# Kernel tuning notes

Measured on AMD Instinct MI355X. Metric: run time of the kernel, lower is better.

Reference implementation:

```python
import jax, jax.numpy as jnp
import numpy as np

N_NODES = 10000
N_EDGES = 160000
IN_CH = 256
HIDDEN = 512
N_LAYERS = 2
W_SCALE = 0.05  # keep relu chain numerically tame


def setup_inputs() -> dict:
    key = jax.random.key(0)
    ks = jax.random.split(key, 8)
    x = jax.random.normal(ks[0], (N_NODES, IN_CH), dtype=jnp.float32)
    edge_index = jax.random.randint(ks[1], (2, N_EDGES), 0, N_NODES, dtype=jnp.int64)
    W_in = jax.random.normal(ks[2], (IN_CH, HIDDEN), dtype=jnp.float32) * W_SCALE
    b_in = jnp.zeros((HIDDEN,), jnp.float32)
    msg_W = jax.random.normal(ks[3], (N_LAYERS, HIDDEN, HIDDEN), dtype=jnp.float32) * W_SCALE
    msg_b = jnp.zeros((N_LAYERS, HIDDEN), jnp.float32)
    upd_W = jax.random.normal(ks[4], (N_LAYERS, 2 * HIDDEN, HIDDEN), dtype=jnp.float32) * W_SCALE
    upd_b = jnp.zeros((N_LAYERS, HIDDEN), jnp.float32)
    W_out = jax.random.normal(ks[5], (HIDDEN, 1), dtype=jnp.float32) * W_SCALE
    b_out = jnp.zeros((1,), jnp.float32)
    return {"x": x, "edge_index": edge_index, "W_in": W_in, "b_in": b_in,
            "msg_W": msg_W, "msg_b": msg_b, "upd_W": upd_W, "upd_b": upd_b,
            "W_out": W_out, "b_out": b_out}


def reference(x, edge_index, W_in, b_in, msg_W, msg_b, upd_W, upd_b, W_out, b_out):
    src = edge_index[0]  # x_j source nodes (PyG source_to_target flow)
    dst = edge_index[1]  # aggregate into destination nodes
    n = x.shape[0]
    h = jax.nn.relu(x @ W_in + b_in)  # [N, H]
    for l in range(msg_W.shape[0]):
        # message: relu(Linear(x_j)) on gathered source features  [E, H]
        m = jax.nn.relu(h[src] @ msg_W[l] + msg_b[l])
        # aggr='add': scatter-add over destination nodes  [N, H]
        aggr = jax.ops.segment_sum(m, dst, num_segments=n)
        # update: relu(Linear(concat([x, aggr])))  [N, H]
        h = jax.nn.relu(jnp.concatenate([h, aggr], axis=-1) @ upd_W[l] + upd_b[l])
    out = h @ W_out + b_out  # [N, 1]
    return out.squeeze(-1)
```

## Files before the change

kernel.cpp:

```cpp
#include <hip/hip_runtime.h>


typedef _Float16 half8 __attribute__((ext_vector_type(8)));
typedef float float4v __attribute__((ext_vector_type(4)));

#define ASYNC_COPY16(gptr, lptr)                                              \
    __builtin_amdgcn_global_load_lds(                                         \
        (const __attribute__((address_space(1))) void*)(gptr),                \
        (__attribute__((address_space(3))) void*)(lptr), 16, 0, 0)


__device__ __forceinline__ void gemm_body(int id,
    const _Float16* __restrict__ A1, int KT1,
    const _Float16* __restrict__ A2, int KT2,
    const _Float16* __restrict__ Wt, int KTw, int ktw2,
    const float* __restrict__ bias, _Float16* __restrict__ C,
    int M, int Mtiles, int packC, int do_relu,
    const float* __restrict__ Wout, const float* __restrict__ bout,
    float* __restrict__ outp)
{
    __shared__ _Float16 As[4096];
    __shared__ _Float16 Bs[4096];

    const int tid  = threadIdx.x;
    const int wave = tid >> 6, lane = tid & 63;

    const int cxcd = id & 7, j = id >> 3;
    const int mt = cxcd + 8 * (j >> 3);
    if (mt >= Mtiles) return;
    const int pn = j & 7;
    const int bm = mt * 64, bn = pn * 64;

    const int wr = (wave >> 1) * 32, wc = (wave & 1) * 32;
    const int m16 = lane & 15, quad = lane >> 4;

    float4v acc[2][2] = {};
    float bv[2];
    #pragma unroll
    for (int jj = 0; jj < 2; ++jj) bv[jj] = bias[bn + wc + jj * 16 + m16];

    for (int pass = 0; pass < 2; ++pass) {
        const _Float16* __restrict__ A = pass ? A2 : A1;
        if (A == nullptr) continue;
        const int KTa  = pass ? KT2 : KT1;
        const int ktw0 = pass ? ktw2 : 0;

        for (int kt = 0; kt < KTa; ++kt) {
            const _Float16* Ab = A  + (size_t)(mt * KTa + kt) * 4096;
            const _Float16* Wb = Wt + (size_t)(pn * KTw + ktw0 + kt) * 4096;
            #pragma unroll
            for (int t = 0; t < 2; ++t) {
                const int q = t * 4 + wave;
                ASYNC_COPY16(Ab + q * 512 + lane * 8, (char*)As + q * 1024);
                ASYNC_COPY16(Wb + q * 512 + lane * 8, (char*)Bs + q * 1024);
            }
            __syncthreads();
            #pragma unroll
            for (int c = 0; c < 2; ++c) {
                half8 af[2], bf[2];
                #pragma unroll
                for (int i2 = 0; i2 < 2; ++i2)
                    af[i2] = *(const half8*)
                        &As[((c * 4 + quad) * 64 + wr + i2 * 16 + m16) * 8];
                #pragma unroll
                for (int j2 = 0; j2 < 2; ++j2)
                    bf[j2] = *(const half8*)
                        &Bs[((c * 4 + quad) * 64 + wc + j2 * 16 + m16) * 8];
                #pragma unroll
                for (int i2 = 0; i2 < 2; ++i2)
                    #pragma unroll
                    for (int j2 = 0; j2 < 2; ++j2)
                        acc[i2][j2] = __builtin_amdgcn_mfma_f32_16x16x32_f16(
                            af[i2], bf[j2], acc[i2][j2], 0, 0, 0);
            }
            __syncthreads();
        }
    }

    if (outp) {
        #pragma unroll
        for (int i = 0; i < 2; ++i)
            #pragma unroll
            for (int rg = 0; rg < 4; ++rg) {
                const int r2 = wr + i * 16 + quad * 4 + rg;
                const int row = bm + r2;
                float pr = 0.f;
                #pragma unroll
                for (int j2 = 0; j2 < 2; ++j2) {
                    float v = fmaxf(acc[i][j2][rg] + bv[j2], 0.f);
                    pr += v * Wout[bn + wc + j2 * 16 + m16];
                }
                pr += __shfl_xor(pr, 1);
                pr += __shfl_xor(pr, 2);
                pr += __shfl_xor(pr, 4);
                pr += __shfl_xor(pr, 8);
                if (m16 == 0 && row < M)
                    atomicAdd(&outp[row],
                              pr + ((pn == 0 && wc == 0) ? bout[0] : 0.f));
            }
        return;
    }

    #pragma unroll
    for (int i = 0; i < 2; ++i)
        #pragma unroll
        for (int rg = 0; rg < 4; ++rg) {
            const int r2 = wr + i * 16 + quad * 4 + rg;
            const int row = bm + r2;
            if (row >= M) continue;
            #pragma unroll
            for (int j2 = 0; j2 < 2; ++j2) {
                float v = acc[i][j2][rg] + bv[j2];
                if (do_relu) v = fmaxf(v, 0.f);
                const int coff = wc + j2 * 16 + m16;
                if (packC) {
                    C[(size_t)((mt * 8 + pn) * 8 + (coff >> 3)) * 512
                      + r2 * 8 + (coff & 7)] = (_Float16)v;
                } else {
                    C[(size_t)row * 512 + bn + coff] = (_Float16)v;
                }
            }
        }
}

__global__ __launch_bounds__(256) void gemm_f16(
    const _Float16* __restrict__ A1, int KT1,
    const _Float16* __restrict__ A2, int KT2,
    const _Float16* __restrict__ Wt, int KTw, int ktw2,
    const float* __restrict__ bias, _Float16* __restrict__ C,
    int M, int Mtiles, int packC, int do_relu,
    const float* Wout, const float* bout, float* outp)
{
    gemm_body(blockIdx.x, A1, KT1, A2, KT2, Wt, KTw, ktw2,
              bias, C, M, Mtiles, packC, do_relu, Wout, bout, outp);
}

__device__ __forceinline__ void transpose_unit(
    const float* __restrict__ src, _Float16* __restrict__ dst, int R, int tb)
{
    const int rtiles = R >> 5;
    const int r0 = (tb % rtiles) * 32, c0 = (tb / rtiles) * 32;
    const int KT = R >> 6;
    __shared__ float t[32][33];
    const int tid = threadIdx.x;
    const int tx = tid & 31, ty = tid >> 5;
    #pragma unroll
    for (int i = 0; i < 32; i += 8)
        t[ty + i][tx] = src[(size_t)(r0 + ty + i) * 512 + c0 + tx];
    __syncthreads();
    if (tid < 128) {
        const int n  = c0 + (tid >> 2);
        const int k0 = r0 + (tid & 3) * 8;
        half8 o;
        #pragma unroll
        for (int j2 = 0; j2 < 8; ++j2)
            o[j2] = (_Float16)t[(tid & 3) * 8 + j2][tid >> 2];
        *(half8*)&dst[(size_t)(((n >> 6) * KT + (k0 >> 6)) * 8 + ((k0 >> 3) & 7)) * 512
                      + (n & 63) * 8] = o;
    }
}

__global__ __launch_bounds__(256) void fill_ingemm(
    const int* __restrict__ eidx, int* __restrict__ cursor,
    int* __restrict__ srcs, int E,
    const _Float16* __restrict__ xb, const _Float16* __restrict__ WinT,
    const float* __restrict__ b_in, _Float16* __restrict__ B0,
    int M, int Mtiles,
    const float* __restrict__ msg_W, _Float16* __restrict__ msgT,
    const float* __restrict__ upd_W, _Float16* __restrict__ updT)
{
    const int gemmU = ((Mtiles + 7) >> 3) * 64;
    const int fillU = (E + 255) >> 8;
    const int b = blockIdx.x;
    if (b < gemmU) {
        gemm_body(b, xb, 4, nullptr, 0, WinT, 4, 0,
                  b_in, B0, M, Mtiles, 1, 1, nullptr, nullptr, nullptr);
        return;
    }
    if (b < gemmU + fillU) {
        const int e = (b - gemmU) * 256 + threadIdx.x;
        if (e < E) {
            const int d = eidx[E + e];
            const int pos = atomicAdd(&cursor[d], 1);
            if (pos < 64) srcs[d * 64 + pos] = eidx[e];
        }
        return;
    }
    const int tB = b - gemmU - fillU;
    if (tB < 256)       transpose_unit(msg_W,              msgT,              512,  tB);
    else if (tB < 512)  transpose_unit(msg_W + 512 * 512,  msgT + 512 * 512,  512,  tB - 256);
    else if (tB < 1024) transpose_unit(upd_W,              updT,              1024, tB - 512);
    else                transpose_unit(upd_W + 1024 * 512, updT + 512 * 1024, 1024, tB - 1024);
}

__global__ __launch_bounds__(256) void prep(
    const float* __restrict__ W_in,  _Float16* __restrict__ WinT,
    const float* __restrict__ x,     _Float16* __restrict__ xb,
    int* __restrict__ cursor, float* __restrict__ outz,
    int n4, int M)
{
    const int b = blockIdx.x;
    const int tid = threadIdx.x;
    const int castU = (n4 + 255) >> 8;
    if (b < 128) {
        transpose_unit(W_in, WinT, 256, b);
    } else if (b < 128 + castU) {
        const int i = (b - 128) * 256 + tid;
        if (i < n4) {
            const float4 v = *(const float4*)(x + (size_t)i * 4);
            ushort4 s;
            union { _Float16 h; unsigned short u; } cv;
            cv.h = (_Float16)v.x; s.x = cv.u;
            cv.h = (_Float16)v.y; s.y = cv.u;
            cv.h = (_Float16)v.z; s.z = cv.u;
            cv.h = (_Float16)v.w; s.w = cv.u;
            const int f = i * 4;
            const int m = f >> 8, k = f & 255;
            *(ushort4*)((unsigned short*)xb
                + (size_t)(((m >> 6) * 4 + (k >> 6)) * 8 + ((k >> 3) & 7)) * 512
                + (m & 63) * 8 + (k & 7)) = s;
        }
    } else {
        const int zi = (b - 128 - castU) * 256 + tid;
        if (zi < M) { cursor[zi] = 0; outz[zi] = 0.f; }
    }
}

__global__ __launch_bounds__(256) void aggregate_f16(
    const _Float16* __restrict__ hmr, const int* __restrict__ cursor,
    const int* __restrict__ srcs, _Float16* __restrict__ ag, int n)
{
    const int l16  = threadIdx.x & 15;
    const int node = blockIdx.x * 16 + (threadIdx.x >> 4);
    if (node >= n) return;
    const int c8 = blockIdx.y * 128 + l16 * 8;
    const int beg = node * 64;
    const int end = beg + min(cursor[node], 64);
    float a[8] = {};
    int j = beg;
    for (; j + 3 < end; j += 4) {
        const half8 v0 = *(const half8*)(hmr + (size_t)srcs[j]     * 512 + c8);
        const half8 v1 = *(const half8*)(hmr + (size_t)srcs[j + 1] * 512 + c8);
        const half8 v2 = *(const half8*)(hmr + (size_t)srcs[j + 2] * 512 + c8);
        const half8 v3 = *(const half8*)(hmr + (size_t)srcs[j + 3] * 512 + c8);
        #pragma unroll
        for (int i = 0; i < 8; ++i)
            a[i] += ((float)v0[i] + (float)v1[i]) + ((float)v2[i] + (float)v3[i]);
    }
    for (; j < end; ++j) {
        const half8 v = *(const half8*)(hmr + (size_t)srcs[j] * 512 + c8);
        #pragma unroll
        for (int i = 0; i < 8; ++i) a[i] += (float)v[i];
    }
    half8 o;
    #pragma unroll
    for (int i = 0; i < 8; ++i) o[i] = (_Float16)a[i];
    *(half8*)(ag + (size_t)(((node >> 6) * 8 + (c8 >> 6)) * 8 + ((c8 >> 3) & 7)) * 512
              + (node & 63) * 8) = o;
}

extern "C" void kernel_launch(void* const* d_in, const int* in_sizes, int n_in,
                              void* d_out, int out_size, void* d_ws, size_t ws_size,
                              hipStream_t stream)
{
    const float* x     = (const float*)d_in[0];
    const int*   eidx  = (const int*)  d_in[1];
    const float* W_in  = (const float*)d_in[2];
    const float* b_in  = (const float*)d_in[3];
    const float* msg_W = (const float*)d_in[4];
    const float* msg_b = (const float*)d_in[5];
    const float* upd_W = (const float*)d_in[6];
    const float* upd_b = (const float*)d_in[7];
    const float* W_out = (const float*)d_in[8];
    const float* b_out = (const float*)d_in[9];

    const int IN = 256, H = 512;
    const int M = in_sizes[0] / IN;
    const int E = in_sizes[1] / 2;
    const int Mtiles = (M + 63) / 64;
    const size_t Mt64 = (size_t)Mtiles * 64;

    _Float16* xb   = (_Float16*)d_ws;
    _Float16* B0   = xb + Mt64 * IN;
    _Float16* B1   = B0 + Mt64 * H;
    _Float16* B2   = B1 + Mt64 * H;
    _Float16* WinT = B2 + Mt64 * H;
    _Float16* msgT = WinT + (size_t)H * IN;
    _Float16* updT = msgT + (size_t)2 * H * H;
    int* cursor = (int*)(updT + (size_t)2 * H * 2 * H);
    int* srcs   = cursor + M;

    const dim3 blk(256);
    const int gemmBlocks = ((Mtiles + 7) / 8) * 64;
    const dim3 aggrGrid((M + 15) / 16, 4);

    const int n4 = M * IN / 4;
    const int castU = (n4 + 255) / 256;
    const int fillU = (E + 255) / 256;
    const int zeroU = (M + 255) / 256;
    const int transU = 1536;

    prep<<<dim3(128 + castU + zeroU), blk, 0, stream>>>(
        W_in, WinT, x, xb, cursor, (float*)d_out, n4, M);
    fill_ingemm<<<dim3(gemmBlocks + fillU + transU), blk, 0, stream>>>(
        eidx, cursor, srcs, E, xb, WinT, b_in, B0, M, Mtiles,
        msg_W, msgT, upd_W, updT);

    gemm_f16<<<dim3(gemmBlocks), blk, 0, stream>>>(B0, 8, nullptr, 0,
        msgT, 8, 0, msg_b, B1, M, Mtiles, 0, 1,
        nullptr, nullptr, nullptr);
    aggregate_f16<<<aggrGrid, blk, 0, stream>>>(B1, cursor, srcs, B2, M);
    gemm_f16<<<dim3(gemmBlocks), blk, 0, stream>>>(B0, 8, B2, 8,
        updT, 16, 8, upd_b, B1, M, Mtiles, 1, 1,
        nullptr, nullptr, nullptr);
    gemm_f16<<<dim3(gemmBlocks), blk, 0, stream>>>(B1, 8, nullptr, 0,
        msgT + 512 * 512, 8, 0, msg_b + 512, B0, M, Mtiles, 0, 1,
        nullptr, nullptr, nullptr);
    aggregate_f16<<<aggrGrid, blk, 0, stream>>>(B0, cursor, srcs, B2, M);
    gemm_f16<<<dim3(gemmBlocks), blk, 0, stream>>>(B1, 8, B2, 8,
        updT + 512 * 1024, 16, 8, upd_b + 512, nullptr, M, Mtiles, 1, 1,
        W_out, b_out, (float*)d_out);
}
```

Measured before the change: 201.3 us.

## Grow GEMM tile to 128x64 and XOR-swizzle packed fp16 layout

The GEMM block tile doubles from 64x64 to 128x64, with each wave computing 32x64 so every B fragment is reused across more rows. All producers of the packed tile layout (transpose, x cast, aggregation, GEMM packed output) now XOR-swizzle the row index by the k-chunk to cut LDS bank conflicts on fragment reads. The aim is less LDS traffic and more MFMA work per byte loaded. In exchange it doubles the accumulator registers and A LDS footprint, halves the number of blocks, and drops the row<M bound check on packed stores, which depends on padded buffers.

```diff
diff --git a/kernel.cpp b/kernel.cpp
--- a/kernel.cpp
+++ b/kernel.cpp
@@ -19,7 +19,7 @@
     const float* __restrict__ Wout, const float* __restrict__ bout,
     float* __restrict__ outp)
 {
-    __shared__ _Float16 As[4096];
+    __shared__ _Float16 As[8192];
     __shared__ _Float16 Bs[4096];
 
     const int tid  = threadIdx.x;
@@ -29,15 +29,17 @@
     const int mt = cxcd + 8 * (j >> 3);
     if (mt >= Mtiles) return;
     const int pn = j & 7;
-    const int bm = mt * 64, bn = pn * 64;
-
-    const int wr = (wave >> 1) * 32, wc = (wave & 1) * 32;
+    const int bm = mt * 128, bn = pn * 64;
+
+    const int wr  = wave * 32;
     const int m16 = lane & 15, quad = lane >> 4;
-
-    float4v acc[2][2] = {};
-    float bv[2];
+    const int sub = wave >> 1;
+    const int rb  = (wave & 1) * 32;
+
+    float4v acc[2][4] = {};
+    float bv[4];
     #pragma unroll
-    for (int jj = 0; jj < 2; ++jj) bv[jj] = bias[bn + wc + jj * 16 + m16];
+    for (int jj = 0; jj < 4; ++jj) bv[jj] = bias[bn + jj * 16 + m16];
 
     for (int pass = 0; pass < 2; ++pass) {
         const _Float16* __restrict__ A = pass ? A2 : A1;
@@ -46,30 +48,33 @@
         const int ktw0 = pass ? ktw2 : 0;
 
         for (int kt = 0; kt < KTa; ++kt) {
-            const _Float16* Ab = A  + (size_t)(mt * KTa + kt) * 4096;
-            const _Float16* Wb = Wt + (size_t)(pn * KTw + ktw0 + kt) * 4096;
+            const _Float16* Ab0 = A + (size_t)((2 * mt)     * KTa + kt) * 4096;
+            const _Float16* Ab1 = A + (size_t)((2 * mt + 1) * KTa + kt) * 4096;
+            const _Float16* Wb  = Wt + (size_t)(pn * KTw + ktw0 + kt) * 4096;
             #pragma unroll
             for (int t = 0; t < 2; ++t) {
                 const int q = t * 4 + wave;
-                ASYNC_COPY16(Ab + q * 512 + lane * 8, (char*)As + q * 1024);
-                ASYNC_COPY16(Wb + q * 512 + lane * 8, (char*)Bs + q * 1024);
+                ASYNC_COPY16(Ab0 + q * 512 + lane * 8, (char*)As + q * 1024);
+                ASYNC_COPY16(Ab1 + q * 512 + lane * 8, (char*)As + 8192 + q * 1024);
+                ASYNC_COPY16(Wb  + q * 512 + lane * 8, (char*)Bs + q * 1024);
             }
             __syncthreads();
             #pragma unroll
             for (int c = 0; c < 2; ++c) {
-                half8 af[2], bf[2];
+                const int ch = c * 4 + quad;
+                half8 af[2], bf[4];
                 #pragma unroll
                 for (int i2 = 0; i2 < 2; ++i2)
                     af[i2] = *(const half8*)
-                        &As[((c * 4 + quad) * 64 + wr + i2 * 16 + m16) * 8];
+                        &As[sub * 4096 + (ch * 64 + ((rb + i2 * 16 + m16) ^ ch)) * 8];
                 #pragma unroll
-                for (int j2 = 0; j2 < 2; ++j2)
+                for (int j2 = 0; j2 < 4; ++j2)
                     bf[j2] = *(const half8*)
-                        &Bs[((c * 4 + quad) * 64 + wc + j2 * 16 + m16) * 8];
+                        &Bs[(ch * 64 + ((j2 * 16 + m16) ^ ch)) * 8];
                 #pragma unroll
                 for (int i2 = 0; i2 < 2; ++i2)
                     #pragma unroll
-                    for (int j2 = 0; j2 < 2; ++j2)
+                    for (int j2 = 0; j2 < 4; ++j2)
                         acc[i2][j2] = __builtin_amdgcn_mfma_f32_16x16x32_f16(
                             af[i2], bf[j2], acc[i2][j2], 0, 0, 0);
             }
@@ -86,17 +91,16 @@
                 const int row = bm + r2;
                 float pr = 0.f;
                 #pragma unroll
-                for (int j2 = 0; j2 < 2; ++j2) {
+                for (int j2 = 0; j2 < 4; ++j2) {
                     float v = fmaxf(acc[i][j2][rg] + bv[j2], 0.f);
-                    pr += v * Wout[bn + wc + j2 * 16 + m16];
+                    pr += v * Wout[bn + j2 * 16 + m16];
                 }
                 pr += __shfl_xor(pr, 1);
                 pr += __shfl_xor(pr, 2);
                 pr += __shfl_xor(pr, 4);
                 pr += __shfl_xor(pr, 8);
                 if (m16 == 0 && row < M)
-                    atomicAdd(&outp[row],
-                              pr + ((pn == 0 && wc == 0) ? bout[0] : 0.f));
+                    atomicAdd(&outp[row], pr + (pn == 0 ? bout[0] : 0.f));
             }
         return;
     }
@@ -107,15 +111,14 @@
         for (int rg = 0; rg < 4; ++rg) {
             const int r2 = wr + i * 16 + quad * 4 + rg;
             const int row = bm + r2;
-            if (row >= M) continue;
             #pragma unroll
-            for (int j2 = 0; j2 < 2; ++j2) {
+            for (int j2 = 0; j2 < 4; ++j2) {
                 float v = acc[i][j2][rg] + bv[j2];
                 if (do_relu) v = fmaxf(v, 0.f);
-                const int coff = wc + j2 * 16 + m16;
+                const int coff = j2 * 16 + m16;
                 if (packC) {
-                    C[(size_t)((mt * 8 + pn) * 8 + (coff >> 3)) * 512
-                      + r2 * 8 + (coff & 7)] = (_Float16)v;
+                    C[(size_t)(((mt * 2 + (r2 >> 6)) * 8 + pn) * 8 + (coff >> 3)) * 512
+                      + ((r2 & 63) ^ (coff >> 3)) * 8 + (coff & 7)] = (_Float16)v;
                 } else {
                     C[(size_t)row * 512 + bn + coff] = (_Float16)v;
                 }
@@ -156,7 +159,7 @@
         for (int j2 = 0; j2 < 8; ++j2)
             o[j2] = (_Float16)t[(tid & 3) * 8 + j2][tid >> 2];
         *(half8*)&dst[(size_t)(((n >> 6) * KT + (k0 >> 6)) * 8 + ((k0 >> 3) & 7)) * 512
-                      + (n & 63) * 8] = o;
+                      + ((n & 63) ^ ((k0 >> 3) & 7)) * 8] = o;
     }
 }
 
@@ -218,7 +221,7 @@
             const int m = f >> 8, k = f & 255;
             *(ushort4*)((unsigned short*)xb
                 + (size_t)(((m >> 6) * 4 + (k >> 6)) * 8 + ((k >> 3) & 7)) * 512
-                + (m & 63) * 8 + (k & 7)) = s;
+                + ((m & 63) ^ ((k >> 3) & 7)) * 8 + (k & 7)) = s;
         }
     } else {
         const int zi = (b - 128 - castU) * 256 + tid;
@@ -256,7 +259,7 @@
     #pragma unroll
     for (int i = 0; i < 8; ++i) o[i] = (_Float16)a[i];
     *(half8*)(ag + (size_t)(((node >> 6) * 8 + (c8 >> 6)) * 8 + ((c8 >> 3) & 7)) * 512
-              + (node & 63) * 8) = o;
+              + ((node & 63) ^ ((c8 >> 3) & 7)) * 8) = o;
 }
 
 extern "C" void kernel_launch(void* const* d_in, const int* in_sizes, int n_in,
@@ -277,14 +280,14 @@
     const int IN = 256, H = 512;
     const int M = in_sizes[0] / IN;
     const int E = in_sizes[1] / 2;
-    const int Mtiles = (M + 63) / 64;
-    const size_t Mt64 = (size_t)Mtiles * 64;
+    const int Mtiles = (M + 127) / 128;
+    const size_t Mt = (size_t)Mtiles * 128;
 
     _Float16* xb   = (_Float16*)d_ws;
-    _Float16* B0   = xb + Mt64 * IN;
-    _Float16* B1   = B0 + Mt64 * H;
-    _Float16* B2   = B1 + Mt64 * H;
-    _Float16* WinT = B2 + Mt64 * H;
+    _Float16* B0   = xb + Mt * IN;
+    _Float16* B1   = B0 + Mt * H;
+    _Float16* B2   = B1 + Mt * H;
+    _Float16* WinT = B2 + Mt * H;
     _Float16* msgT = WinT + (size_t)H * IN;
     _Float16* updT = msgT + (size_t)2 * H * H;
     int* cursor = (int*)(updT + (size_t)2 * H * 2 * H);
```

Measured after the change: 204.7 us. About the same (+1.7%).

## Double-buffer LDS tiles in GEMM to overlap async loads with MFMA

Applied to the files above, without the earlier changes.

Doubles the LDS A/B buffers and restructures the K loop so the next tile's async global-to-LDS copies are issued before computing on the current tile, waiting on vmcnt(4) so only the older loads must land. The two-pass loop over A1/A2 is flattened into one unified tile index. This targets the exposed global load latency at every K step, at the cost of twice the LDS per block, which may reduce occupancy, and of relying on hand-written waitcnt counts.

```diff
diff --git a/kernel.cpp b/kernel.cpp
--- a/kernel.cpp
+++ b/kernel.cpp
@@ -19,8 +19,8 @@
     const float* __restrict__ Wout, const float* __restrict__ bout,
     float* __restrict__ outp)
 {
-    __shared__ _Float16 As[4096];
-    __shared__ _Float16 Bs[4096];
+    __shared__ _Float16 As[8192];
+    __shared__ _Float16 Bs[8192];
 
     const int tid  = threadIdx.x;
     const int wave = tid >> 6, lane = tid & 63;
@@ -39,42 +39,60 @@
     #pragma unroll
     for (int jj = 0; jj < 2; ++jj) bv[jj] = bias[bn + wc + jj * 16 + m16];
 
-    for (int pass = 0; pass < 2; ++pass) {
-        const _Float16* __restrict__ A = pass ? A2 : A1;
-        if (A == nullptr) continue;
-        const int KTa  = pass ? KT2 : KT1;
-        const int ktw0 = pass ? ktw2 : 0;
-
-        for (int kt = 0; kt < KTa; ++kt) {
-            const _Float16* Ab = A  + (size_t)(mt * KTa + kt) * 4096;
-            const _Float16* Wb = Wt + (size_t)(pn * KTw + ktw0 + kt) * 4096;
-            #pragma unroll
-            for (int t = 0; t < 2; ++t) {
-                const int q = t * 4 + wave;
-                ASYNC_COPY16(Ab + q * 512 + lane * 8, (char*)As + q * 1024);
-                ASYNC_COPY16(Wb + q * 512 + lane * 8, (char*)Bs + q * 1024);
-            }
-            __syncthreads();
-            #pragma unroll
-            for (int c = 0; c < 2; ++c) {
-                half8 af[2], bf[2];
-                #pragma unroll
-                for (int i2 = 0; i2 < 2; ++i2)
-                    af[i2] = *(const half8*)
-                        &As[((c * 4 + quad) * 64 + wr + i2 * 16 + m16) * 8];
+    const int total = KT1 + (A2 ? KT2 : 0);
+
+    auto stageT = [&](int t, int buf) {
+        const _Float16* __restrict__ A;
+        int KTa, kt;
+        if (t < KT1) { A = A1; KTa = KT1; kt = t; }
+        else         { A = A2; KTa = KT2; kt = t - KT1; }
+        const int ktw = (t < KT1) ? t : ktw2 + (t - KT1);
+        const _Float16* Ab = A  + (size_t)(mt * KTa + kt) * 4096;
+        const _Float16* Wb = Wt + (size_t)(pn * KTw + ktw) * 4096;
+        #pragma unroll
+        for (int t2 = 0; t2 < 2; ++t2) {
+            const int q = t2 * 4 + wave;
+            ASYNC_COPY16(Ab + q * 512 + lane * 8,
+                         (char*)As + buf * 8192 + q * 1024);
+            ASYNC_COPY16(Wb + q * 512 + lane * 8,
+                         (char*)Bs + buf * 8192 + q * 1024);
+        }
+    };
+
+    auto computeT = [&](int buf) {
+        #pragma unroll
+        for (int c = 0; c < 2; ++c) {
+            half8 af[2], bf[2];
+            #pragma unroll
+            for (int i2 = 0; i2 < 2; ++i2)
+                af[i2] = *(const half8*)
+                    &As[buf * 4096 + ((c * 4 + quad) * 64 + wr + i2 * 16 + m16) * 8];
+            #pragma unroll
+            for (int j2 = 0; j2 < 2; ++j2)
+                bf[j2] = *(const half8*)
+                    &Bs[buf * 4096 + ((c * 4 + quad) * 64 + wc + j2 * 16 + m16) * 8];
+            #pragma unroll
+            for (int i2 = 0; i2 < 2; ++i2)
                 #pragma unroll
                 for (int j2 = 0; j2 < 2; ++j2)
-                    bf[j2] = *(const half8*)
-                        &Bs[((c * 4 + quad) * 64 + wc + j2 * 16 + m16) * 8];
-                #pragma unroll
-                for (int i2 = 0; i2 < 2; ++i2)
-                    #pragma unroll
-                    for (int j2 = 0; j2 < 2; ++j2)
-                        acc[i2][j2] = __builtin_amdgcn_mfma_f32_16x16x32_f16(
-                            af[i2], bf[j2], acc[i2][j2], 0, 0, 0);
-            }
-            __syncthreads();
-        }
+                    acc[i2][j2] = __builtin_amdgcn_mfma_f32_16x16x32_f16(
+                        af[i2], bf[j2], acc[i2][j2], 0, 0, 0);
+        }
+    };
+
+    stageT(0, 0);
+    for (int t = 0; t < total; ++t) {
+        if (t + 1 < total) {
+            stageT(t + 1, (t + 1) & 1);
+            asm volatile("s_waitcnt vmcnt(4)" ::: "memory");
+        } else {
+            asm volatile("s_waitcnt vmcnt(0)" ::: "memory");
+        }
+        __builtin_amdgcn_s_barrier();
+        __builtin_amdgcn_sched_barrier(0);
+        computeT(t & 1);
+        __builtin_amdgcn_s_barrier();
+        __builtin_amdgcn_sched_barrier(0);
     }
 
     if (outp) {
```

Measured after the change: 222.2 us. 10.4% more time.

## Fuse message GEMM with self-half of update GEMM sharing A tile loads

Applied to the files above, without the earlier changes.

Adds a dual-output GEMM that reads h once and computes both the message linear layer and the h-part of the update linear layer, storing the latter as an fp16 partial buffer. The update GEMM then starts its accumulators from that partial and only runs over the aggregated half of K. This removes a second read of h from global memory and halves the update GEMM's K loop. In exchange the dual kernel uses more LDS and registers, which may lower occupancy, and the fp16 partial adds a write/read plus a rounding step.

```diff
diff --git a/kernel.cpp b/kernel.cpp
--- a/kernel.cpp
+++ b/kernel.cpp
@@ -16,6 +16,7 @@
     const _Float16* __restrict__ Wt, int KTw, int ktw2,
     const float* __restrict__ bias, _Float16* __restrict__ C,
     int M, int Mtiles, int packC, int do_relu,
+    const _Float16* __restrict__ Pin,
     const float* __restrict__ Wout, const float* __restrict__ bout,
     float* __restrict__ outp)
 {
@@ -35,6 +36,17 @@
     const int m16 = lane & 15, quad = lane >> 4;
 
     float4v acc[2][2] = {};
+    if (Pin) {
+        const _Float16* Pt = Pin + (size_t)(mt * 8 + pn) * 4096
+                                 + wave * 64 + lane;
+        #pragma unroll
+        for (int i = 0; i < 2; ++i)
+            #pragma unroll
+            for (int j2 = 0; j2 < 2; ++j2)
+                #pragma unroll
+                for (int rg = 0; rg < 4; ++rg)
+                    acc[i][j2][rg] = (float)Pt[((i * 2 + j2) * 4 + rg) * 256];
+    }
     float bv[2];
     #pragma unroll
     for (int jj = 0; jj < 2; ++jj) bv[jj] = bias[bn + wc + jj * 16 + m16];
@@ -129,10 +141,105 @@
     const _Float16* __restrict__ Wt, int KTw, int ktw2,
     const float* __restrict__ bias, _Float16* __restrict__ C,
     int M, int Mtiles, int packC, int do_relu,
+    const _Float16* Pin,
     const float* Wout, const float* bout, float* outp)
 {
     gemm_body(blockIdx.x, A1, KT1, A2, KT2, Wt, KTw, ktw2,
-              bias, C, M, Mtiles, packC, do_relu, Wout, bout, outp);
+              bias, C, M, Mtiles, packC, do_relu, Pin, Wout, bout, outp);
+}
+
+__global__ __launch_bounds__(256) void gemm_dual(
+    const _Float16* __restrict__ A,
+    const _Float16* __restrict__ W1,
+    const _Float16* __restrict__ W2,
+    const float* __restrict__ b1,
+    _Float16* __restrict__ C1,
+    _Float16* __restrict__ P,
+    int M, int Mtiles)
+{
+    __shared__ _Float16 As[4096];
+    __shared__ _Float16 B1s[4096];
+    __shared__ _Float16 B2s[4096];
+
+    const int id = blockIdx.x;
+    const int tid  = threadIdx.x;
+    const int wave = tid >> 6, lane = tid & 63;
+
+    const int cxcd = id & 7, j = id >> 3;
+    const int mt = cxcd + 8 * (j >> 3);
+    if (mt >= Mtiles) return;
+    const int pn = j & 7;
+    const int bm = mt * 64, bn = pn * 64;
+
+    const int wr = (wave >> 1) * 32, wc = (wave & 1) * 32;
+    const int m16 = lane & 15, quad = lane >> 4;
+
+    float4v accM[2][2] = {};
+    float4v accP[2][2] = {};
+    float bv[2];
+    #pragma unroll
+    for (int jj = 0; jj < 2; ++jj) bv[jj] = b1[bn + wc + jj * 16 + m16];
+
+    for (int kt = 0; kt < 8; ++kt) {
+        const _Float16* Ab  = A  + (size_t)(mt * 8  + kt) * 4096;
+        const _Float16* W1b = W1 + (size_t)(pn * 8  + kt) * 4096;
+        const _Float16* W2b = W2 + (size_t)(pn * 16 + kt) * 4096;
+        #pragma unroll
+        for (int t = 0; t < 2; ++t) {
+            const int q = t * 4 + wave;
+            ASYNC_COPY16(Ab  + q * 512 + lane * 8, (char*)As  + q * 1024);
+            ASYNC_COPY16(W1b + q * 512 + lane * 8, (char*)B1s + q * 1024);
+            ASYNC_COPY16(W2b + q * 512 + lane * 8, (char*)B2s + q * 1024);
+        }
+        __syncthreads();
+        #pragma unroll
+        for (int c = 0; c < 2; ++c) {
+            half8 af[2], b1f[2], b2f[2];
+            #pragma unroll
+            for (int i2 = 0; i2 < 2; ++i2)
+                af[i2] = *(const half8*)
+                    &As[((c * 4 + quad) * 64 + wr + i2 * 16 + m16) * 8];
+            #pragma unroll
+            for (int j2 = 0; j2 < 2; ++j2) {
+                b1f[j2] = *(const half8*)
+                    &B1s[((c * 4 + quad) * 64 + wc + j2 * 16 + m16) * 8];
+                b2f[j2] = *(const half8*)
+                    &B2s[((c * 4 + quad) * 64 + wc + j2 * 16 + m16) * 8];
+            }
+            #pragma unroll
+            for (int i2 = 0; i2 < 2; ++i2)
+                #pragma unroll
+                for (int j2 = 0; j2 < 2; ++j2) {
+                    accM[i2][j2] = __builtin_amdgcn_mfma_f32_16x16x32_f16(
+                        af[i2], b1f[j2], accM[i2][j2], 0, 0, 0);
+                    accP[i2][j2] = __builtin_amdgcn_mfma_f32_16x16x32_f16(
+                        af[i2], b2f[j2], accP[i2][j2], 0, 0, 0);
+                }
+        }
+        __syncthreads();
+    }
+
+    #pragma unroll
+    for (int i = 0; i < 2; ++i)
+        #pragma unroll
+        for (int rg = 0; rg < 4; ++rg) {
+            const int r2 = wr + i * 16 + quad * 4 + rg;
+            const int row = bm + r2;
+            if (row >= M) continue;
+            #pragma unroll
+            for (int j2 = 0; j2 < 2; ++j2) {
+                float v = fmaxf(accM[i][j2][rg] + bv[j2], 0.f);
+                C1[(size_t)row * 512 + bn + wc + j2 * 16 + m16] = (_Float16)v;
+            }
+        }
+    _Float16* Pt = P + (size_t)(mt * 8 + pn) * 4096 + wave * 64 + lane;
+    #pragma unroll
+    for (int i = 0; i < 2; ++i)
+        #pragma unroll
+        for (int j2 = 0; j2 < 2; ++j2)
+            #pragma unroll
+            for (int rg = 0; rg < 4; ++rg)
+                Pt[((i * 2 + j2) * 4 + rg) * 256] = (_Float16)accP[i][j2][rg];
 }
 
 __device__ __forceinline__ void transpose_unit(
@@ -174,7 +281,7 @@
     const int b = blockIdx.x;
     if (b < gemmU) {
         gemm_body(b, xb, 4, nullptr, 0, WinT, 4, 0,
-                  b_in, B0, M, Mtiles, 1, 1, nullptr, nullptr, nullptr);
+                  b_in, B0, M, Mtiles, 1, 1, nullptr, nullptr, nullptr, nullptr);
         return;
     }
     if (b < gemmU + fillU) {
@@ -289,6 +396,7 @@
     _Float16* updT = msgT + (size_t)2 * H * H;
     int* cursor = (int*)(updT + (size_t)2 * H * 2 * H);
     int* srcs   = cursor + M;
+    _Float16* Pbuf = (_Float16*)(srcs + (size_t)M * 64);
 
     const dim3 blk(256);
     const int gemmBlocks = ((Mtiles + 7) / 8) * 64;
@@ -306,18 +414,17 @@
         eidx, cursor, srcs, E, xb, WinT, b_in, B0, M, Mtiles,
         msg_W, msgT, upd_W, updT);
 
-    gemm_f16<<<dim3(gemmBlocks), blk, 0, stream>>>(B0, 8, nullptr, 0,
-        msgT, 8, 0, msg_b, B1, M, Mtiles, 0, 1,
-        nullptr, nullptr, nullptr);
+    gemm_dual<<<dim3(gemmBlocks), blk, 0, stream>>>(
+        B0, msgT, updT, msg_b, B1, Pbuf, M, Mtiles);
     aggregate_f16<<<aggrGrid, blk, 0, stream>>>(B1, cursor, srcs, B2, M);
-    gemm_f16<<<dim3(gemmBlocks), blk, 0, stream>>>(B0, 8, B2, 8,
+    gemm_f16<<<dim3(gemmBlocks), blk, 0, stream>>>(nullptr, 0, B2, 8,
         updT, 16, 8, upd_b, B1, M, Mtiles, 1, 1,
-        nullptr, nullptr, nullptr);
-    gemm_f16<<<dim3(gemmBlocks), blk, 0, stream>>>(B1, 8, nullptr, 0,
-        msgT + 512 * 512, 8, 0, msg_b + 512, B0, M, Mtiles, 0, 1,
-        nullptr, nullptr, nullptr);
+        Pbuf, nullptr, nullptr, nullptr);
+    gemm_dual<<<dim3(gemmBlocks), blk, 0, stream>>>(
+        B1, msgT + 512 * 512, updT + 512 * 1024, msg_b + 512,
+        B0, Pbuf, M, Mtiles);
     aggregate_f16<<<aggrGrid, blk, 0, stream>>>(B0, cursor, srcs, B2, M);
-    gemm_f16<<<dim3(gemmBlocks), blk, 0, stream>>>(B1, 8, B2, 8,
+    gemm_f16<<<dim3(gemmBlocks), blk, 0, stream>>>(nullptr, 0, B2, 8,
         updT + 512 * 1024, 16, 8, upd_b + 512, nullptr, M, Mtiles, 1, 1,
-        W_out, b_out, (float*)d_out);
-}
+        Pbuf, W_out, b_out, (float*)d_out);
+}
```

New measurement: 198.5 us. No clear change (-1.4%).
